# Optimization experiments

Hardware: AMD Instinct MI355X
Metric: run time of the kernel (lower is better)

## Reference

```python
import jax, jax.numpy as jnp
import numpy as np

N_NODES = 200_000
N_EDGES = 6_400_000
N_GRAPHS = 512


def _graph_conv(x, src, dst, W_rel, b_rel, W_root, n_nodes):
    # PyG GraphConv (aggr='add'): lin_rel(sum_{j->i} x_j) + lin_root(x_i)
    agg = jax.ops.segment_sum(x[src], dst, num_segments=n_nodes)  # [N, in]
    return agg @ W_rel.T + b_rel + x @ W_root.T


def setup_inputs() -> dict:
    key = jax.random.key(0)
    ks = jax.random.split(key, 12)
    x = jax.random.normal(ks[0], (N_NODES, 3), dtype=jnp.float32)
    edge_index = jax.random.randint(ks[1], (2, N_EDGES), 0, N_NODES, dtype=jnp.int64)
    batch = jnp.sort(jax.random.randint(ks[2], (N_NODES,), 0, N_GRAPHS, dtype=jnp.int64))

    def xavier(k, shape):
        fan_out, fan_in = shape
        lim = np.sqrt(6.0 / (fan_in + fan_out)).astype(np.float32)
        return jax.random.uniform(k, shape, jnp.float32, -lim, lim)

    return {
        "x": x, "edge_index": edge_index, "batch": batch,
        "W1_rel": xavier(ks[3], (32, 3)),  "b1": jnp.zeros((32,), jnp.float32), "W1_root": xavier(ks[4], (32, 3)),
        "W2_rel": xavier(ks[5], (16, 32)), "b2": jnp.zeros((16,), jnp.float32), "W2_root": xavier(ks[6], (16, 32)),
        "W3_rel": xavier(ks[7], (8, 16)),  "b3": jnp.zeros((8,), jnp.float32),  "W3_root": xavier(ks[8], (8, 16)),
        "W_lin": xavier(ks[9], (1, 8)),    "b_lin": jnp.zeros((1,), jnp.float32),
    }


def reference(x, edge_index, batch,
              W1_rel, b1, W1_root,
              W2_rel, b2, W2_root,
              W3_rel, b3, W3_root,
              W_lin, b_lin):
    src, dst = edge_index[0], edge_index[1]
    h = jax.nn.relu(_graph_conv(x, src, dst, W1_rel, b1, W1_root, N_NODES))
    h = jax.nn.relu(_graph_conv(h, src, dst, W2_rel, b2, W2_root, N_NODES))
    h = jax.nn.relu(_graph_conv(h, src, dst, W3_rel, b3, W3_root, N_NODES))
    pooled = jax.ops.segment_max(h, batch, num_segments=N_GRAPHS)  # [G, 8]
    out = pooled @ W_lin.T + b_lin  # [G, 1]
    return out[:, 0]
```

## Files before the change

kernel.cpp:

```cpp
#include <hip/hip_runtime.h>
#include <hip/hip_fp16.h>

#define N_NODES 200000
#define N_EDGES 6400000
#define N_GRAPHS 512

#define NB 3125
#define CHUNK 4096
#define NCH 1563
#define NGRP 25
#define CPG 63
#define SEG 13
#define SCAP 3072

typedef float vf4 __attribute__((ext_vector_type(4)));
typedef float vf2 __attribute__((ext_vector_type(2)));
typedef unsigned vu2 __attribute__((ext_vector_type(2)));

__device__ __forceinline__ unsigned ntload_u(const unsigned* p) {
  return __builtin_nontemporal_load(p);
}
__device__ __forceinline__ int ntload_i(const int* p) { return __builtin_nontemporal_load(p); }
__device__ __forceinline__ float ntload_f(const float* p) {
  return __builtin_nontemporal_load(p);
}
__device__ __forceinline__ float2 ntload_f2(const float* p) {
  vf2 v = __builtin_nontemporal_load((const vf2*)p);
  return make_float2(v.x, v.y);
}
__device__ __forceinline__ void ntstore_u2(unsigned* p, uint2 v) {
  vu2 t = {v.x, v.y};
  __builtin_nontemporal_store(t, (vu2*)p);
}
__device__ __forceinline__ void ntstore_f2(float* p, float2 v) {
  vf2 t = {v.x, v.y};
  __builtin_nontemporal_store(t, (vf2*)p);
}
__device__ __forceinline__ void ntstore_f4(float* p, float4 v) {
  vf4 t = {v.x, v.y, v.z, v.w};
  __builtin_nontemporal_store(t, (vf4*)p);
}
__device__ __forceinline__ void ntstore_u(unsigned* p, unsigned v) {
  __builtin_nontemporal_store(v, p);
}


__global__ __launch_bounds__(256) void count_kernel(const int* __restrict__ dst,
                                                    unsigned short* __restrict__ H) {
  __shared__ unsigned hist[NB];
  for (int i = threadIdx.x; i < NB; i += 256) hist[i] = 0;
  __syncthreads();
  int c = blockIdx.x;
  long e0 = (long)c * CHUNK;
  long rem = (long)N_EDGES - e0;
  int n = rem > CHUNK ? CHUNK : (int)rem;
  for (int i = threadIdx.x; i < n; i += 256) atomicAdd(&hist[dst[e0 + i] >> 6], 1u);
  __syncthreads();
  for (int i = threadIdx.x; i < NB; i += 256) H[(size_t)c * NB + i] = (unsigned short)hist[i];
}

__global__ __launch_bounds__(256) void scan_bins1_kernel(unsigned short* __restrict__ H,
                                                         unsigned* __restrict__ P) {
  int b = blockIdx.x * 256 + threadIdx.x;
  int g = blockIdx.y;
  if (b >= NB) return;
  int c0 = g * CPG, c1 = min(NCH, (g + 1) * CPG);
  unsigned run = 0;
  for (int c = c0; c < c1; c++) {
    unsigned t = H[(size_t)c * NB + b];
    H[(size_t)c * NB + b] = (unsigned short)run;
    run += t;
  }
  P[(size_t)g * NB + b] = run;
}

__global__ __launch_bounds__(256) void scan_bins2_kernel(unsigned* __restrict__ P,
                                                         unsigned* __restrict__ bucketTotal) {
  int b = blockIdx.x * 256 + threadIdx.x;
  if (b >= NB) return;
  unsigned run = 0;
  for (int g = 0; g < NGRP; g++) {
    unsigned t = P[(size_t)g * NB + b];
    P[(size_t)g * NB + b] = run;
    run += t;
  }
  bucketTotal[b] = run;
}

__global__ __launch_bounds__(256) void scan_total_kernel(const unsigned* __restrict__ bucketTotal,
                                                         unsigned* __restrict__ bucketStart) {
  __shared__ unsigned sv[256 * SEG];
  __shared__ unsigned partial[256];
  int t = threadIdx.x;
  for (int i = t; i < 256 * SEG; i += 256) sv[i] = (i < NB) ? bucketTotal[i] : 0u;
  __syncthreads();
  unsigned sum = 0;
#pragma unroll
  for (int k = 0; k < SEG; k++) sum += sv[t * SEG + k];
  partial[t] = sum;
  __syncthreads();
  for (int off = 1; off < 256; off <<= 1) {
    unsigned add = (t >= off) ? partial[t - off] : 0u;
    __syncthreads();
    partial[t] += add;
    __syncthreads();
  }
  unsigned run = partial[t] - sum;
#pragma unroll
  for (int k = 0; k < SEG; k++) {
    unsigned w = sv[t * SEG + k];
    sv[t * SEG + k] = run;
    run += w;
  }
  __syncthreads();
  for (int i = t; i < NB; i += 256) bucketStart[i] = sv[i];
  if (t == 0) bucketStart[NB] = N_EDGES;
}

__global__ __launch_bounds__(256) void scatter_sorted_kernel(
    const int* __restrict__ src, const int* __restrict__ dst,
    const unsigned short* __restrict__ H, const unsigned* __restrict__ P,
    const unsigned* __restrict__ bucketStart, unsigned* __restrict__ packed) {
  __shared__ unsigned ssort[CHUNK];
  __shared__ unsigned short sbort[CHUNK];
  __shared__ unsigned hist[3328];
  __shared__ unsigned cur[3328];
  __shared__ unsigned partial[256];
  int t = threadIdx.x;
  int c = blockIdx.x;
  int g = c / CPG;
  long e0 = (long)c * CHUNK;
  long rem = (long)N_EDGES - e0;
  int n = rem > CHUNK ? CHUNK : (int)rem;
  for (int i = t; i < 3328; i += 256) hist[i] = 0;
  __syncthreads();
  for (int i = t; i < n; i += 256) atomicAdd(&hist[dst[e0 + i] >> 6], 1u);
  __syncthreads();
  unsigned a[SEG], sum = 0;
#pragma unroll
  for (int k = 0; k < SEG; k++) { a[k] = hist[SEG * t + k]; sum += a[k]; }
  partial[t] = sum;
  __syncthreads();
  for (int off = 1; off < 256; off <<= 1) {
    unsigned add = (t >= off) ? partial[t - off] : 0u;
    __syncthreads();
    partial[t] += add;
    __syncthreads();
  }
  unsigned run = partial[t] - sum;
#pragma unroll
  for (int k = 0; k < SEG; k++) {
    hist[SEG * t + k] = run;
    cur[SEG * t + k] = run;
    run += a[k];
  }
  __syncthreads();
  for (int i = t; i < n; i += 256) {
    int d = dst[e0 + i], s = src[e0 + i];
    int b = d >> 6;
    unsigned r = atomicAdd(&cur[b], 1u);
    ssort[r] = ((unsigned)s << 7) | (unsigned)(d & 63);
    sbort[r] = (unsigned short)b;
  }
  __syncthreads();
  for (int b = t; b < NB; b += 256)
    cur[b] = bucketStart[b] + P[(size_t)g * NB + b] + H[(size_t)c * NB + b] - hist[b];
  __syncthreads();
  for (int j = t; j < n; j += 256) packed[cur[sbort[j]] + j] = ssort[j];
}

__global__ __launch_bounds__(256) void sort2_kernel(const unsigned* __restrict__ packedA,
                                                    const unsigned* __restrict__ bucketStart,
                                                    unsigned* __restrict__ packedB,
                                                    unsigned* __restrict__ nodeStart) {
  __shared__ unsigned buf[SCAP];
  __shared__ unsigned buf2[SCAP];
  __shared__ unsigned hist[64], base[64], cur[64];
  int t = threadIdx.x, b = blockIdx.x;
  unsigned s0 = bucketStart[b], s1 = bucketStart[b + 1];
  int n = (int)(s1 - s0);
  if (t < 64) hist[t] = 0;
  for (int i = t; i < n; i += 256) buf[i] = packedA[s0 + i];
  __syncthreads();
  for (int i = t; i < n; i += 256) atomicAdd(&hist[buf[i] & 63u], 1u);
  __syncthreads();
  if (t == 0) {
    unsigned run = 0;
    for (int k = 0; k < 64; k++) {
      unsigned v = hist[k];
      base[k] = run;
      cur[k] = run;
      run += v;
    }
  }
  __syncthreads();
  if (t < 64) nodeStart[b * 64 + t] = s0 + base[t];
  for (int i = t; i < n; i += 256) {
    unsigned p = buf[i];
    unsigned pos = atomicAdd(&cur[p & 63u], 1u);
    buf2[pos] = p >> 7;
  }
  __syncthreads();
  for (int i = t; i < n; i += 256) packedB[s0 + i] = buf2[i];
  if (b == NB - 1 && t == 0) nodeStart[N_NODES] = N_EDGES;
}

__global__ __launch_bounds__(256) void xpad_kernel(const float* __restrict__ x,
                                                   float4* __restrict__ xp) {
  int n = blockIdx.x * 256 + threadIdx.x;
  if (n >= N_NODES) return;
  xp[n] = make_float4(x[3 * n], x[3 * n + 1], x[3 * n + 2], 0.f);
}

__device__ __forceinline__ void half8_unpack(uint4 g, float* f) {
  const __half2* h2 = reinterpret_cast<const __half2*>(&g);
#pragma unroll
  for (int j = 0; j < 4; j++) {
    float2 fj = __half22float2(h2[j]);
    f[2 * j] = fj.x;
    f[2 * j + 1] = fj.y;
  }
}

__global__ __launch_bounds__(256) void layer1_kernel(
    const unsigned* __restrict__ packed, const unsigned* __restrict__ nodeStart,
    const float4* __restrict__ xp,
    const float* __restrict__ W1_rel, const float* __restrict__ b1,
    const float* __restrict__ W1_root,
    const float* __restrict__ W2_rel, const float* __restrict__ W2_root,
    unsigned* __restrict__ t2h, float* __restrict__ r2) {
  __shared__ float sW1rel[96], sW1root[96], sb1[32], sW2rel[512], sW2root[512];
  __shared__ float plds[256 * 4];
  for (int i = threadIdx.x; i < 96; i += 256) { sW1rel[i] = W1_rel[i]; sW1root[i] = W1_root[i]; }
  for (int i = threadIdx.x; i < 32; i += 256) sb1[i] = b1[i];
  for (int i = threadIdx.x; i < 512; i += 256) { sW2rel[i] = W2_rel[i]; sW2root[i] = W2_root[i]; }
  __syncthreads();
  int t = threadIdx.x, ln = t >> 2, part = t & 3;
  int node = blockIdx.x * 64 + ln;
  unsigned s1v = ntload_u(&nodeStart[node + 1]);
  float a0 = 0.f, a1 = 0.f, a2 = 0.f;
  for (unsigned base = ntload_u(&nodeStart[node]) + part; base < s1v; base += 16) {
    unsigned i1 = base + 4, i2 = base + 8, i3 = base + 12;
    unsigned e0 = ntload_u(&packed[base]);
    unsigned e1 = ntload_u(&packed[i1]);
    unsigned e2 = ntload_u(&packed[i2]);
    unsigned e3 = ntload_u(&packed[i3]);
    float4 g0 = xp[e0], g1 = xp[e1], g2 = xp[e2], g3 = xp[e3];
    float m1 = (i1 < s1v) ? 1.f : 0.f;
    float m2 = (i2 < s1v) ? 1.f : 0.f;
    float m3 = (i3 < s1v) ? 1.f : 0.f;
    a0 += g0.x + m1 * g1.x + m2 * g2.x + m3 * g3.x;
    a1 += g0.y + m1 * g1.y + m2 * g2.y + m3 * g3.y;
    a2 += g0.z + m1 * g1.z + m2 * g2.z + m3 * g3.z;
  }
  plds[t * 4] = a0; plds[t * 4 + 1] = a1; plds[t * 4 + 2] = a2;
  __syncthreads();
  int pb = ln * 16;
  float A0 = plds[pb] + plds[pb + 4] + plds[pb + 8] + plds[pb + 12];
  float A1 = plds[pb + 1] + plds[pb + 5] + plds[pb + 9] + plds[pb + 13];
  float A2 = plds[pb + 2] + plds[pb + 6] + plds[pb + 10] + plds[pb + 14];
  float4 xv = xp[node];
  float h[32];
#pragma unroll
  for (int k = 0; k < 32; k++) {
    float v = sW1rel[3 * k] * A0 + sW1rel[3 * k + 1] * A1 + sW1rel[3 * k + 2] * A2 +
              sW1root[3 * k] * xv.x + sW1root[3 * k + 1] * xv.y + sW1root[3 * k + 2] * xv.z +
              sb1[k];
    h[k] = fmaxf(v, 0.f);
  }
  int jb = part * 4;
  float tv[4], rv[4];
#pragma unroll
  for (int j = 0; j < 4; j++) {
    float acc = 0.f, accr = 0.f;
#pragma unroll
    for (int k = 0; k < 32; k++) {
      acc += sW2rel[32 * (jb + j) + k] * h[k];
      accr += sW2root[32 * (jb + j) + k] * h[k];
    }
    tv[j] = acc;
    rv[j] = accr;
  }
  __half2 p0 = __halves2half2(__float2half_rn(tv[0]), __float2half_rn(tv[1]));
  __half2 p1 = __halves2half2(__float2half_rn(tv[2]), __float2half_rn(tv[3]));
  ntstore_u2(&t2h[(size_t)node * 8 + part * 2], make_uint2(*(unsigned*)&p0, *(unsigned*)&p1));
  ntstore_f4(&r2[(size_t)node * 16 + jb], make_float4(rv[0], rv[1], rv[2], rv[3]));
}

__global__ __launch_bounds__(256) void layer2_kernel(
    const unsigned* __restrict__ packed, const unsigned* __restrict__ nodeStart,
    const uint4* __restrict__ t2h4, const float* __restrict__ r2,
    const float* __restrict__ b2,
    const float* __restrict__ W3_rel, const float* __restrict__ W3_root,
    unsigned* __restrict__ t3h, float* __restrict__ r3) {
  __shared__ float sW3rel[128], sW3root[128], sb2[16];
  __shared__ float plds[256 * 9];
  __shared__ float hlds[32 * 16];
  for (int i = threadIdx.x; i < 128; i += 256) { sW3rel[i] = W3_rel[i]; sW3root[i] = W3_root[i]; }
  if (threadIdx.x < 16) sb2[threadIdx.x] = b2[threadIdx.x];
  __syncthreads();
  int t = threadIdx.x, ln = t >> 3, p = t & 7;
  int node = blockIdx.x * 32 + ln;
  int half = p & 1;
  unsigned s1v = ntload_u(&nodeStart[node + 1]);
  float acc[8];
#pragma unroll
  for (int j = 0; j < 8; j++) acc[j] = 0.f;
  for (unsigned base = ntload_u(&nodeStart[node]) + (p >> 1); base < s1v; base += 16) {
    unsigned i1 = base + 4, i2 = base + 8, i3 = base + 12;
    unsigned e0 = ntload_u(&packed[base]);
    unsigned e1 = ntload_u(&packed[i1]);
    unsigned e2 = ntload_u(&packed[i2]);
    unsigned e3 = ntload_u(&packed[i3]);
    uint4 g0 = t2h4[(size_t)e0 * 2 + half];
    uint4 g1 = t2h4[(size_t)e1 * 2 + half];
    uint4 g2 = t2h4[(size_t)e2 * 2 + half];
    uint4 g3 = t2h4[(size_t)e3 * 2 + half];
    float m1 = (i1 < s1v) ? 1.f : 0.f;
    float m2 = (i2 < s1v) ? 1.f : 0.f;
    float m3 = (i3 < s1v) ? 1.f : 0.f;
    float f0[8], f1[8], f2[8], f3[8];
    half8_unpack(g0, f0);
    half8_unpack(g1, f1);
    half8_unpack(g2, f2);
    half8_unpack(g3, f3);
#pragma unroll
    for (int j = 0; j < 8; j++)
      acc[j] += f0[j] + m1 * f1[j] + m2 * f2[j] + m3 * f3[j];
  }
#pragma unroll
  for (int j = 0; j < 8; j++) plds[t * 9 + j] = acc[j];
  __syncthreads();
  {
    float2 rv = ntload_f2(&r2[(size_t)node * 16 + 2 * p]);
    float hv[2];
#pragma unroll
    for (int k2 = 0; k2 < 2; k2++) {
      int f = 2 * p + k2;
      int fh = f >> 3, fi = f & 7;
      int q0 = (ln * 8 + fh) * 9 + fi;
      float s = plds[q0] + plds[q0 + 18] + plds[q0 + 36] + plds[q0 + 54];
      hv[k2] = s + sb2[f] + (k2 == 0 ? rv.x : rv.y);
    }
    hlds[ln * 16 + 2 * p] = fmaxf(hv[0], 0.f);
    hlds[ln * 16 + 2 * p + 1] = fmaxf(hv[1], 0.f);
  }
  __syncthreads();
  const float* W = (p < 4) ? sW3rel : sW3root;
  int rbase = (p < 4) ? 2 * p : 2 * (p - 4);
  float o0 = 0.f, o1 = 0.f;
#pragma unroll
  for (int k = 0; k < 16; k++) {
    float hv = hlds[ln * 16 + k];
    o0 += W[16 * rbase + k] * hv;
    o1 += W[16 * (rbase + 1) + k] * hv;
  }
  if (p < 4) {
    __half2 pk = __halves2half2(__float2half_rn(o0), __float2half_rn(o1));
    ntstore_u(&t3h[(size_t)node * 4 + p], *(unsigned*)&pk);
  } else {
    ntstore_f2(&r3[(size_t)node * 8 + rbase], make_float2(o0, o1));
  }
}

__global__ __launch_bounds__(256) void layer3_kernel(
    const unsigned* __restrict__ packed, const unsigned* __restrict__ nodeStart,
    const uint4* __restrict__ t3h4, const float* __restrict__ r3,
    const float* __restrict__ b3,
    const int* __restrict__ batch, unsigned* __restrict__ pooled) {
  __shared__ float plds[256 * 9];
  __shared__ float sb3[8];
  if (threadIdx.x < 8) sb3[threadIdx.x] = b3[threadIdx.x];
  __syncthreads();
  int t = threadIdx.x, ln = t >> 3, p = t & 7;
  int node = blockIdx.x * 32 + ln;
  unsigned s1v = ntload_u(&nodeStart[node + 1]);
  float acc[8];
#pragma unroll
  for (int j = 0; j < 8; j++) acc[j] = 0.f;
  for (unsigned base = ntload_u(&nodeStart[node]) + p; base < s1v; base += 32) {
    unsigned i1 = base + 8, i2 = base + 16, i3 = base + 24;
    unsigned e0 = ntload_u(&packed[base]);
    unsigned e1 = ntload_u(&packed[i1]);
    unsigned e2 = ntload_u(&packed[i2]);
    unsigned e3 = ntload_u(&packed[i3]);
    uint4 g0 = t3h4[e0];
    uint4 g1 = t3h4[e1];
    uint4 g2 = t3h4[e2];
    uint4 g3 = t3h4[e3];
    float m1 = (i1 < s1v) ? 1.f : 0.f;
    float m2 = (i2 < s1v) ? 1.f : 0.f;
    float m3 = (i3 < s1v) ? 1.f : 0.f;
    float f0[8], f1[8], f2[8], f3[8];
    half8_unpack(g0, f0);
    half8_unpack(g1, f1);
    half8_unpack(g2, f2);
    half8_unpack(g3, f3);
#pragma unroll
    for (int j = 0; j < 8; j++)
      acc[j] += f0[j] + m1 * f1[j] + m2 * f2[j] + m3 * f3[j];
  }
#pragma unroll
  for (int j = 0; j < 8; j++) plds[t * 9 + j] = acc[j];
  __syncthreads();
  int gg = ntload_i(&batch[node]);
  int q0 = ln * 72 + p;
  float v = plds[q0] + plds[q0 + 9] + plds[q0 + 18] + plds[q0 + 27] +
            plds[q0 + 36] + plds[q0 + 45] + plds[q0 + 54] + plds[q0 + 63];
  float h = fmaxf(v + sb3[p] + ntload_f(&r3[(size_t)node * 8 + p]), 0.f);
  atomicMax(&pooled[8 * gg + p], __float_as_uint(h));
}

__global__ __launch_bounds__(256) void final_kernel(
    const unsigned* __restrict__ pooled, const float* __restrict__ W_lin,
    const float* __restrict__ b_lin, float* __restrict__ out) {
  int g = blockIdx.x * blockDim.x + threadIdx.x;
  if (g >= N_GRAPHS) return;
  float acc = b_lin[0];
#pragma unroll
  for (int f = 0; f < 8; f++) acc += __uint_as_float(pooled[8 * g + f]) * W_lin[f];
  out[g] = acc;
}

extern "C" void kernel_launch(void* const* d_in, const int* in_sizes, int n_in,
                              void* d_out, int out_size, void* d_ws, size_t ws_size,
                              hipStream_t stream) {
  const float* x = (const float*)d_in[0];
  const int* ei = (const int*)d_in[1];
  const int* src = ei;
  const int* dst = ei + N_EDGES;
  const int* batch = (const int*)d_in[2];
  const float* W1_rel = (const float*)d_in[3];
  const float* b1 = (const float*)d_in[4];
  const float* W1_root = (const float*)d_in[5];
  const float* W2_rel = (const float*)d_in[6];
  const float* b2 = (const float*)d_in[7];
  const float* W2_root = (const float*)d_in[8];
  const float* W3_rel = (const float*)d_in[9];
  const float* b3 = (const float*)d_in[10];
  const float* W3_root = (const float*)d_in[11];
  const float* W_lin = (const float*)d_in[12];
  const float* b_lin = (const float*)d_in[13];
  float* out = (float*)d_out;

  char* ws = (char*)d_ws;
  unsigned* packedA = (unsigned*)(ws + 0);
  float* r2 = (float*)(ws + 0);
  float* r3 = (float*)(ws + 12800000);
  unsigned* t3h = (unsigned*)(ws + 19200000);
  float4* xpad = (float4*)(ws + 22400000);
  unsigned short* H = (unsigned short*)(ws + 25600000);
  unsigned* packedB = (unsigned*)(ws + 25600000);
  unsigned* t2h = (unsigned*)(ws + 51200128);
  unsigned* pooled = (unsigned*)(ws + 57600128);
  unsigned* bucketStart = (unsigned*)(ws + 57616512);
  unsigned* bucketTotal = (unsigned*)(ws + 57629016);
  unsigned* P = (unsigned*)(ws + 57641516);
  unsigned* nodeStart = (unsigned*)(ws + 57954016);

  hipMemsetAsync(pooled, 0, N_GRAPHS * 8 * sizeof(unsigned), stream);
  hipMemsetAsync(packedB + N_EDGES, 0, 128, stream);

  count_kernel<<<NCH, 256, 0, stream>>>(dst, H);
  scan_bins1_kernel<<<dim3((NB + 255) / 256, NGRP), 256, 0, stream>>>(H, P);
  scan_bins2_kernel<<<(NB + 255) / 256, 256, 0, stream>>>(P, bucketTotal);
  scan_total_kernel<<<1, 256, 0, stream>>>(bucketTotal, bucketStart);
  scatter_sorted_kernel<<<NCH, 256, 0, stream>>>(src, dst, H, P, bucketStart, packedA);
  sort2_kernel<<<NB, 256, 0, stream>>>(packedA, bucketStart, packedB, nodeStart);
  xpad_kernel<<<(N_NODES + 255) / 256, 256, 0, stream>>>(x, xpad);

  layer1_kernel<<<NB, 256, 0, stream>>>(packedB, nodeStart, xpad,
                                        W1_rel, b1, W1_root, W2_rel, W2_root, t2h, r2);
  layer2_kernel<<<N_NODES / 32, 256, 0, stream>>>(packedB, nodeStart, (const uint4*)t2h, r2, b2,
                                                  W3_rel, W3_root, t3h, r3);
  layer3_kernel<<<N_NODES / 32, 256, 0, stream>>>(packedB, nodeStart, (const uint4*)t3h, r3, b3,
                                                  batch, pooled);
  final_kernel<<<(N_GRAPHS + 255) / 256, 256, 0, stream>>>(pooled, W_lin, b_lin, out);
}
```

Baseline: 506.2 us.

## Stage per-block edge lists in LDS and remap threads in gather kernels

Each layer kernel now loads its block's contiguous CSR edge slice into shared memory with coalesced loads, then the per-node loops read source indices from LDS instead of issuing scattered global loads. Layer2 switches each thread to gather both 16-byte halves of a node row, with 8 threads per node striding by 32. Layer3 moves to 64 nodes per block with 4 threads per node, and its epilogue now computes two features per thread. Shared-memory use rises, which can lower occupancy. Correctness relies on a block's edge count fitting in the fixed ECAP capacities, with no fallback when a block has more edges.

```diff
diff --git a/kernel.cpp b/kernel.cpp
--- a/kernel.cpp
+++ b/kernel.cpp
@@ -12,6 +12,8 @@
 #define CPG 63
 #define SEG 13
 #define SCAP 3072
+#define ECAP64 2816
+#define ECAP32 1536
 
 typedef float vf4 __attribute__((ext_vector_type(4)));
 typedef float vf2 __attribute__((ext_vector_type(2)));
@@ -230,21 +232,29 @@
     const float* __restrict__ W2_rel, const float* __restrict__ W2_root,
     unsigned* __restrict__ t2h, float* __restrict__ r2) {
   __shared__ float sW1rel[96], sW1root[96], sb1[32], sW2rel[512], sW2root[512];
+  __shared__ unsigned sedge[ECAP64];
+  __shared__ unsigned snode[65];
   __shared__ float plds[256 * 4];
-  for (int i = threadIdx.x; i < 96; i += 256) { sW1rel[i] = W1_rel[i]; sW1root[i] = W1_root[i]; }
-  for (int i = threadIdx.x; i < 32; i += 256) sb1[i] = b1[i];
-  for (int i = threadIdx.x; i < 512; i += 256) { sW2rel[i] = W2_rel[i]; sW2root[i] = W2_root[i]; }
-  __syncthreads();
-  int t = threadIdx.x, ln = t >> 2, part = t & 3;
-  int node = blockIdx.x * 64 + ln;
-  unsigned s1v = ntload_u(&nodeStart[node + 1]);
+  int t = threadIdx.x, blk = blockIdx.x;
+  for (int i = t; i < 96; i += 256) { sW1rel[i] = W1_rel[i]; sW1root[i] = W1_root[i]; }
+  for (int i = t; i < 32; i += 256) sb1[i] = b1[i];
+  for (int i = t; i < 512; i += 256) { sW2rel[i] = W2_rel[i]; sW2root[i] = W2_root[i]; }
+  if (t < 65) snode[t] = ntload_u(&nodeStart[blk * 64 + t]);
+  __syncthreads();
+  unsigned ebase = snode[0];
+  int nE = (int)(snode[64] - ebase);
+  for (int i = t; i < nE; i += 256) sedge[i] = ntload_u(&packed[ebase + i]);
+  __syncthreads();
+  int ln = t >> 2, part = t & 3;
+  int node = blk * 64 + ln;
+  unsigned s1v = snode[ln + 1] - ebase;
   float a0 = 0.f, a1 = 0.f, a2 = 0.f;
-  for (unsigned base = ntload_u(&nodeStart[node]) + part; base < s1v; base += 16) {
-    unsigned i1 = base + 4, i2 = base + 8, i3 = base + 12;
-    unsigned e0 = ntload_u(&packed[base]);
-    unsigned e1 = ntload_u(&packed[i1]);
-    unsigned e2 = ntload_u(&packed[i2]);
-    unsigned e3 = ntload_u(&packed[i3]);
+  for (unsigned u = snode[ln] - ebase + part; u < s1v; u += 16) {
+    unsigned i1 = u + 4, i2 = u + 8, i3 = u + 12;
+    unsigned e0 = sedge[u];
+    unsigned e1 = sedge[(i1 < s1v) ? i1 : u];
+    unsigned e2 = sedge[(i2 < s1v) ? i2 : u];
+    unsigned e3 = sedge[(i3 < s1v) ? i3 : u];
     float4 g0 = xp[e0], g1 = xp[e1], g2 = xp[e2], g3 = xp[e3];
     float m1 = (i1 < s1v) ? 1.f : 0.f;
     float m2 = (i2 < s1v) ? 1.f : 0.f;
@@ -294,42 +304,50 @@
     const float* __restrict__ W3_rel, const float* __restrict__ W3_root,
     unsigned* __restrict__ t3h, float* __restrict__ r3) {
   __shared__ float sW3rel[128], sW3root[128], sb2[16];
-  __shared__ float plds[256 * 9];
+  __shared__ unsigned sedge[ECAP32];
+  __shared__ unsigned snode[33];
+  __shared__ float plds[256 * 17];
   __shared__ float hlds[32 * 16];
-  for (int i = threadIdx.x; i < 128; i += 256) { sW3rel[i] = W3_rel[i]; sW3root[i] = W3_root[i]; }
-  if (threadIdx.x < 16) sb2[threadIdx.x] = b2[threadIdx.x];
-  __syncthreads();
-  int t = threadIdx.x, ln = t >> 3, p = t & 7;
-  int node = blockIdx.x * 32 + ln;
-  int half = p & 1;
-  unsigned s1v = ntload_u(&nodeStart[node + 1]);
-  float acc[8];
-#pragma unroll
-  for (int j = 0; j < 8; j++) acc[j] = 0.f;
-  for (unsigned base = ntload_u(&nodeStart[node]) + (p >> 1); base < s1v; base += 16) {
-    unsigned i1 = base + 4, i2 = base + 8, i3 = base + 12;
-    unsigned e0 = ntload_u(&packed[base]);
-    unsigned e1 = ntload_u(&packed[i1]);
-    unsigned e2 = ntload_u(&packed[i2]);
-    unsigned e3 = ntload_u(&packed[i3]);
-    uint4 g0 = t2h4[(size_t)e0 * 2 + half];
-    uint4 g1 = t2h4[(size_t)e1 * 2 + half];
-    uint4 g2 = t2h4[(size_t)e2 * 2 + half];
-    uint4 g3 = t2h4[(size_t)e3 * 2 + half];
+  int t = threadIdx.x, blk = blockIdx.x;
+  for (int i = t; i < 128; i += 256) { sW3rel[i] = W3_rel[i]; sW3root[i] = W3_root[i]; }
+  if (t < 16) sb2[t] = b2[t];
+  if (t < 33) snode[t] = ntload_u(&nodeStart[blk * 32 + t]);
+  __syncthreads();
+  unsigned ebase = snode[0];
+  int nE = (int)(snode[32] - ebase);
+  for (int i = t; i < nE; i += 256) sedge[i] = ntload_u(&packed[ebase + i]);
+  __syncthreads();
+  int ln = t >> 3, p = t & 7;
+  int node = blk * 32 + ln;
+  unsigned s1v = snode[ln + 1] - ebase;
+  float acc[16];
+#pragma unroll
+  for (int j = 0; j < 16; j++) acc[j] = 0.f;
+  for (unsigned u = snode[ln] - ebase + p; u < s1v; u += 32) {
+    unsigned i1 = u + 8, i2 = u + 16, i3 = u + 24;
+    unsigned e0 = sedge[u];
+    unsigned e1 = sedge[(i1 < s1v) ? i1 : u];
+    unsigned e2 = sedge[(i2 < s1v) ? i2 : u];
+    unsigned e3 = sedge[(i3 < s1v) ? i3 : u];
+    uint4 ga0 = t2h4[(size_t)e0 * 2], gb0 = t2h4[(size_t)e0 * 2 + 1];
+    uint4 ga1 = t2h4[(size_t)e1 * 2], gb1 = t2h4[(size_t)e1 * 2 + 1];
+    uint4 ga2 = t2h4[(size_t)e2 * 2], gb2 = t2h4[(size_t)e2 * 2 + 1];
+    uint4 ga3 = t2h4[(size_t)e3 * 2], gb3 = t2h4[(size_t)e3 * 2 + 1];
     float m1 = (i1 < s1v) ? 1.f : 0.f;
     float m2 = (i2 < s1v) ? 1.f : 0.f;
     float m3 = (i3 < s1v) ? 1.f : 0.f;
     float f0[8], f1[8], f2[8], f3[8];
-    half8_unpack(g0, f0);
-    half8_unpack(g1, f1);
-    half8_unpack(g2, f2);
-    half8_unpack(g3, f3);
-#pragma unroll
-    for (int j = 0; j < 8; j++)
-      acc[j] += f0[j] + m1 * f1[j] + m2 * f2[j] + m3 * f3[j];
-  }
-#pragma unroll
-  for (int j = 0; j < 8; j++) plds[t * 9 + j] = acc[j];
+    half8_unpack(ga0, f0); half8_unpack(ga1, f1);
+    half8_unpack(ga2, f2); half8_unpack(ga3, f3);
+#pragma unroll
+    for (int j = 0; j < 8; j++) acc[j] += f0[j] + m1 * f1[j] + m2 * f2[j] + m3 * f3[j];
+    half8_unpack(gb0, f0); half8_unpack(gb1, f1);
+    half8_unpack(gb2, f2); half8_unpack(gb3, f3);
+#pragma unroll
+    for (int j = 0; j < 8; j++) acc[8 + j] += f0[j] + m1 * f1[j] + m2 * f2[j] + m3 * f3[j];
+  }
+#pragma unroll
+  for (int j = 0; j < 16; j++) plds[t * 17 + j] = acc[j];
   __syncthreads();
   {
     float2 rv = ntload_f2(&r2[(size_t)node * 16 + 2 * p]);
@@ -337,9 +355,10 @@
 #pragma unroll
     for (int k2 = 0; k2 < 2; k2++) {
       int f = 2 * p + k2;
-      int fh = f >> 3, fi = f & 7;
-      int q0 = (ln * 8 + fh) * 9 + fi;
-      float s = plds[q0] + plds[q0 + 18] + plds[q0 + 36] + plds[q0 + 54];
+      int q0 = (ln * 8) * 17 + f;
+      float s = 0.f;
+#pragma unroll
+      for (int q = 0; q < 8; q++) s += plds[q0 + q * 17];
       hv[k2] = s + sb2[f] + (k2 == 0 ? rv.x : rv.y);
     }
     hlds[ln * 16 + 2 * p] = fmaxf(hv[0], 0.f);
@@ -368,47 +387,54 @@
     const uint4* __restrict__ t3h4, const float* __restrict__ r3,
     const float* __restrict__ b3,
     const int* __restrict__ batch, unsigned* __restrict__ pooled) {
+  __shared__ unsigned sedge[ECAP64];
+  __shared__ unsigned snode[65];
   __shared__ float plds[256 * 9];
   __shared__ float sb3[8];
-  if (threadIdx.x < 8) sb3[threadIdx.x] = b3[threadIdx.x];
-  __syncthreads();
-  int t = threadIdx.x, ln = t >> 3, p = t & 7;
-  int node = blockIdx.x * 32 + ln;
-  unsigned s1v = ntload_u(&nodeStart[node + 1]);
+  int t = threadIdx.x, blk = blockIdx.x;
+  if (t < 8) sb3[t] = b3[t];
+  if (t < 65) snode[t] = ntload_u(&nodeStart[blk * 64 + t]);
+  __syncthreads();
+  unsigned ebase = snode[0];
+  int nE = (int)(snode[64] - ebase);
+  for (int i = t; i < nE; i += 256) sedge[i] = ntload_u(&packed[ebase + i]);
+  __syncthreads();
+  int ln = t >> 2, p = t & 3;
+  unsigned s1v = snode[ln + 1] - ebase;
   float acc[8];
 #pragma unroll
   for (int j = 0; j < 8; j++) acc[j] = 0.f;
-  for (unsigned base = ntload_u(&nodeStart[node]) + p; base < s1v; base += 32) {
-    unsigned i1 = base + 8, i2 = base + 16, i3 = base + 24;
-    unsigned e0 = ntload_u(&packed[base]);
-    unsigned e1 = ntload_u(&packed[i1]);
-    unsigned e2 = ntload_u(&packed[i2]);
-    unsigned e3 = ntload_u(&packed[i3]);
-    uint4 g0 = t3h4[e0];
-    uint4 g1 = t3h4[e1];
-    uint4 g2 = t3h4[e2];
-    uint4 g3 = t3h4[e3];
+  for (unsigned u = snode[ln] - ebase + p; u < s1v; u += 16) {
+    unsigned i1 = u + 4, i2 = u + 8, i3 = u + 12;
+    unsigned e0 = sedge[u];
+    unsigned e1 = sedge[(i1 < s1v) ? i1 : u];
+    unsigned e2 = sedge[(i2 < s1v) ? i2 : u];
+    unsigned e3 = sedge[(i3 < s1v) ? i3 : u];
+    uint4 g0 = t3h4[e0], g1 = t3h4[e1], g2 = t3h4[e2], g3 = t3h4[e3];
     float m1 = (i1 < s1v) ? 1.f : 0.f;
     float m2 = (i2 < s1v) ? 1.f : 0.f;
     float m3 = (i3 < s1v) ? 1.f : 0.f;
     float f0[8], f1[8], f2[8], f3[8];
-    half8_unpack(g0, f0);
-    half8_unpack(g1, f1);
-    half8_unpack(g2, f2);
-    half8_unpack(g3, f3);
-#pragma unroll
-    for (int j = 0; j < 8; j++)
-      acc[j] += f0[j] + m1 * f1[j] + m2 * f2[j] + m3 * f3[j];
+    half8_unpack(g0, f0); half8_unpack(g1, f1);
+    half8_unpack(g2, f2); half8_unpack(g3, f3);
+#pragma unroll
+    for (int j = 0; j < 8; j++) acc[j] += f0[j] + m1 * f1[j] + m2 * f2[j] + m3 * f3[j];
   }
 #pragma unroll
   for (int j = 0; j < 8; j++) plds[t * 9 + j] = acc[j];
   __syncthreads();
-  int gg = ntload_i(&batch[node]);
-  int q0 = ln * 72 + p;
-  float v = plds[q0] + plds[q0 + 9] + plds[q0 + 18] + plds[q0 + 27] +
-            plds[q0 + 36] + plds[q0 + 45] + plds[q0 + 54] + plds[q0 + 63];
-  float h = fmaxf(v + sb3[p] + ntload_f(&r3[(size_t)node * 8 + p]), 0.f);
-  atomicMax(&pooled[8 * gg + p], __float_as_uint(h));
+  int cn = t >> 2;
+  int node2 = blk * 64 + cn;
+  int f0i = (t & 3) * 2;
+  int gg = ntload_i(&batch[node2]);
+  float2 rv = ntload_f2(&r3[(size_t)node2 * 8 + f0i]);
+  int q0 = cn * 36 + f0i;
+#pragma unroll
+  for (int k2 = 0; k2 < 2; k2++) {
+    float v = plds[q0 + k2] + plds[q0 + 9 + k2] + plds[q0 + 18 + k2] + plds[q0 + 27 + k2];
+    float h = fmaxf(v + sb3[f0i + k2] + (k2 == 0 ? rv.x : rv.y), 0.f);
+    atomicMax(&pooled[8 * gg + f0i + k2], __float_as_uint(h));
+  }
 }
 
 __global__ __launch_bounds__(256) void final_kernel(
@@ -459,7 +485,6 @@
   unsigned* nodeStart = (unsigned*)(ws + 57954016);
 
   hipMemsetAsync(pooled, 0, N_GRAPHS * 8 * sizeof(unsigned), stream);
-  hipMemsetAsync(packedB + N_EDGES, 0, 128, stream);
 
   count_kernel<<<NCH, 256, 0, stream>>>(dst, H);
   scan_bins1_kernel<<<dim3((NB + 255) / 256, NGRP), 256, 0, stream>>>(H, P);
@@ -473,7 +498,7 @@
                                         W1_rel, b1, W1_root, W2_rel, W2_root, t2h, r2);
   layer2_kernel<<<N_NODES / 32, 256, 0, stream>>>(packedB, nodeStart, (const uint4*)t2h, r2, b2,
                                                   W3_rel, W3_root, t3h, r3);
-  layer3_kernel<<<N_NODES / 32, 256, 0, stream>>>(packedB, nodeStart, (const uint4*)t3h, r3, b3,
-                                                  batch, pooled);
+  layer3_kernel<<<NB, 256, 0, stream>>>(packedB, nodeStart, (const uint4*)t3h, r3, b3,
+                                        batch, pooled);
   final_kernel<<<(N_GRAPHS + 255) / 256, 256, 0, stream>>>(pooled, W_lin, b_lin, out);
 }
```

Measured after the change: 539.4 us. 6.6% more time.
